# Optimization experiments

Hardware: AMD Instinct MI355X
Metric: run time of the kernel (lower is better)

## Reference

```python
import jax, jax.numpy as jnp
import numpy as np

FULL_RANGE = 128
MOOD_DIM = 4
LAYERS = 4
UNITS = 512
MOOD_UNITS = 32


def lstm_layer(x, Wih, Whh, bih, bhh):
    # x: [B, T, I]; torch LSTM gate order: i, f, g, o
    B, T, _ = x.shape
    H = Whh.shape[1]
    xg = jnp.einsum('bti,gi->btg', x, Wih) + bih + bhh  # [B, T, 4H]

    def step(carry, g_t):
        h, c = carry
        g = g_t + h @ Whh.T
        i, f, gc, o = jnp.split(g, 4, axis=-1)
        c = jax.nn.sigmoid(f) * c + jax.nn.sigmoid(i) * jnp.tanh(gc)
        h = jax.nn.sigmoid(o) * jnp.tanh(c)
        return (h, c), h

    h0 = jnp.zeros((B, H), x.dtype)
    (_, _), hs = jax.lax.scan(step, (h0, h0), xg.transpose(1, 0, 2))
    return hs.transpose(1, 0, 2)  # [B, T, H]


def setup_inputs() -> dict:
    key = jax.random.key(0)
    ks = jax.random.split(key, 16)
    s = 0.05
    H4 = 4 * UNITS
    in0 = FULL_RANGE + MOOD_UNITS
    return {
        'inputs': jax.random.normal(ks[0], (16, 1024, FULL_RANGE), jnp.float32),
        'moods': jax.random.normal(ks[1], (16, MOOD_DIM), jnp.float32),
        'W_mood': jax.random.normal(ks[2], (MOOD_UNITS, MOOD_DIM), jnp.float32) * s,
        'b_mood': jnp.zeros((MOOD_UNITS,), jnp.float32),
        'W_ih0': jax.random.normal(ks[3], (H4, in0), jnp.float32) * s,
        'W_hh0': jax.random.normal(ks[4], (H4, UNITS), jnp.float32) * s,
        'b_ih0': jax.random.normal(ks[5], (H4,), jnp.float32) * s,
        'b_hh0': jax.random.normal(ks[6], (H4,), jnp.float32) * s,
        'W_ih_rest': jax.random.normal(ks[7], (LAYERS - 1, H4, UNITS), jnp.float32) * s,
        'W_hh_rest': jax.random.normal(ks[8], (LAYERS - 1, H4, UNITS), jnp.float32) * s,
        'b_ih_rest': jax.random.normal(ks[9], (LAYERS - 1, H4), jnp.float32) * s,
        'b_hh_rest': jax.random.normal(ks[10], (LAYERS - 1, H4), jnp.float32) * s,
        'W_out': jax.random.normal(ks[11], (FULL_RANGE, UNITS), jnp.float32) * s,
        'b_out': jnp.zeros((FULL_RANGE,), jnp.float32),
    }


def reference(inputs, moods, W_mood, b_mood, W_ih0, W_hh0, b_ih0, b_hh0,
              W_ih_rest, W_hh_rest, b_ih_rest, b_hh_rest, W_out, b_out):
    B, S, _ = inputs.shape
    m = moods @ W_mood.T + b_mood                      # [B, MOOD_UNITS]
    m = jnp.broadcast_to(m[:, None, :], (B, S, MOOD_UNITS))
    x = jnp.concatenate([inputs, m], axis=2)           # [B, S, FULL_RANGE+MOOD_UNITS]

    params = [(W_ih0, W_hh0, b_ih0, b_hh0)] + [
        (W_ih_rest[i], W_hh_rest[i], b_ih_rest[i], b_hh_rest[i])
        for i in range(LAYERS - 1)
    ]
    for i, (Wih, Whh, bih, bhh) in enumerate(params):
        prev = x
        d = 2 ** i
        F = x.shape[-1]
        # torch unfold(1,d,d).permute(0,3,1,2).view(B*d, S//d, F):
        # sub-batch (b,k) is the stride-d subsequence with phase k
        xd = x.reshape(B, S // d, d, F).transpose(0, 2, 1, 3).reshape(B * d, S // d, F)
        yd = lstm_layer(xd, Wih, Whh, bih, bhh)         # [B*d, S//d, H]
        x = yd.reshape(B, d, S // d, UNITS).transpose(0, 2, 1, 3).reshape(B, S, UNITS)
        if i > 0:
            x = prev + x
    return x @ W_out.T + b_out                          # [B, S, FULL_RANGE]
```

## Files before the change

kernel.cpp:

```cpp
#include <hip/hip_runtime.h>
#include <stdint.h>

#define DEVFN __device__ __forceinline__
#define SCOPE_AGENT __HIP_MEMORY_SCOPE_AGENT

static constexpr int B_ = 16;
static constexpr int S_ = 1024;
static constexpr int FR = 128;
static constexpr int MU = 32;
static constexpr int H_ = 512;
static constexpr int G4 = 2048;

static constexpr int NCH_WHH = 4 * 64 * 2048;
static constexpr int NCH_WI0 = 16 * 2048;
static constexpr int NCH_WIR = 3 * 64 * 2048;
static constexpr int NCH_TOT = NCH_WHH + NCH_WI0 + NCH_WIR;

static constexpr int HV64 = 128 * 256;
static constexpr int NXF = 16 * 16 * 16;

typedef _Float16 h2_t __attribute__((ext_vector_type(2)));

DEVFN uint16_t f2h(float x) { union { _Float16 f; uint16_t u; } c; c.f = (_Float16)x; return c.u; }
DEVFN uint32_t pack_f16(float a, float b) { return (uint32_t)f2h(a) | ((uint32_t)f2h(b) << 16); }

DEVFN float fd2(uint32_t a, uint32_t b, float c) {
#if __has_builtin(__builtin_amdgcn_fdot2)
    return __builtin_amdgcn_fdot2(__builtin_bit_cast(h2_t, a),
                                  __builtin_bit_cast(h2_t, b), c, false);
#else
    asm("v_dot2_f32_f16 %0, %1, %2, %0" : "+v"(c) : "v"(a), "v"(b));
    return c;
#endif
}
DEVFN float dot8f(uint4 w, uint4 x, float s) {
    s = fd2(w.x, x.x, s); s = fd2(w.y, x.y, s);
    s = fd2(w.z, x.z, s); s = fd2(w.w, x.w, s);
    return s;
}
DEVFN float sigm(float x) { return 1.0f / (1.0f + __expf(-x)); }
DEVFN float tanhfast(float x) {
    float e = __expf(2.0f * fabsf(x));
    float r = 1.0f - 2.0f / (e + 1.0f);
    return copysignf(r, x);
}

__global__ __launch_bounds__(256) void mood_kernel(
    const float* __restrict__ moods, const float* __restrict__ W_mood,
    const float* __restrict__ b_mood, const float* __restrict__ W_ih0,
    const float* __restrict__ b_ih0, const float* __restrict__ b_hh0,
    float* __restrict__ mc)
{
    int b = blockIdx.x, tid = threadIdx.x;
    __shared__ float m[MU];
    if (tid < MU) {
        float s = b_mood[tid];
        #pragma unroll
        for (int j = 0; j < 4; j++) s += moods[b * 4 + j] * W_mood[tid * 4 + j];
        m[tid] = s;
    }
    __syncthreads();
    for (int row = tid; row < G4; row += 256) {
        float s = b_ih0[row] + b_hh0[row];
        const float* w = W_ih0 + (size_t)row * (FR + MU) + FR;
        #pragma unroll
        for (int u = 0; u < MU; u++) s += m[u] * w[u];
        mc[(size_t)b * G4 + row] = s;
    }
}

__global__ __launch_bounds__(256) void pack_kernel(
    const float* __restrict__ W_hh0, const float* __restrict__ W_hh_r,
    const float* __restrict__ W_ih0, const float* __restrict__ W_ih_r,
    uint4* __restrict__ pwh, uint4* __restrict__ pwi0, uint4* __restrict__ pwir)
{
    int c = blockIdx.x * 256 + threadIdx.x;
    if (c >= NCH_TOT) return;
    const float* src;
    uint4* dst;
    if (c < NCH_WHH) {
        int l = c >> 17, ck = (c >> 11) & 63, row = c & 2047;
        const float* W = (l == 0) ? W_hh0 : W_hh_r + (size_t)(l - 1) * G4 * H_;
        src = W + (size_t)row * H_ + ck * 8;
        dst = pwh + c;
    } else if (c < NCH_WHH + NCH_WI0) {
        int d = c - NCH_WHH;
        int ck = d >> 11, row = d & 2047;
        src = W_ih0 + (size_t)row * (FR + MU) + ck * 8;
        dst = pwi0 + d;
    } else {
        int e = c - NCH_WHH - NCH_WI0;
        int l = e >> 17, ck = (e >> 11) & 63, row = e & 2047;
        src = W_ih_r + (size_t)l * G4 * H_ + (size_t)row * H_ + ck * 8;
        dst = pwir + e;
    }
    uint4 o;
    o.x = pack_f16(src[0], src[1]);
    o.y = pack_f16(src[2], src[3]);
    o.z = pack_f16(src[4], src[5]);
    o.w = pack_f16(src[6], src[7]);
    *dst = o;
}

#define HSTEP(J) { \
    _Pragma("unroll") \
    for (int b = 0; b < SB; b++) { \
        uint4 hv = *(const uint4*)&lds_h[b * H_ + kg * 64 + (J) * 8]; \
        accA[b] = dot8f(h0c##J, hv, accA[b]); \
        accB[b] = dot8f(h1c##J, hv, accB[b]); \
    } }

#define XBODY(J) { \
    uint4 w0 = WI0[(size_t)(J) * G4 + row0]; \
    uint4 w1 = WI0[(size_t)(J) * G4 + row1]; \
    _Pragma("unroll") \
    for (int b = 0; b < SB; b++) { \
        uint4 xv = *(const uint4*)&lds_x[b * KIN + kg * (KIN / 8) + (J) * 8]; \
        accA[b] = dot8f(w0, xv, accA[b]); \
        accB[b] = dot8f(w1, xv, accB[b]); \
    } }

template <int LAYER>
DEVFN void scan_body(
    int bid, const float* x_in, float* x_out,
    const uint4* __restrict__ pwi, const uint4* __restrict__ pwh,
    const float* __restrict__ biasA, const float* __restrict__ biasB,
    unsigned long long* __restrict__ hb64, uint32_t* __restrict__ xf,
    uint16_t* lds_x, uint16_t* lds_h, float* lds_p, float* lds_res)
{
    constexpr int DIL = 1 << LAYER;
    constexpr int SB = DIL;
    constexpr int T = S_ / DIL;
    constexpr int KIN = (LAYER == 0) ? FR : H_;
    constexpr int NJX = KIN / 64;
    constexpr int XTOT = SB * KIN;
    constexpr int XRS = (XTOT + 511) / 512;
    constexpr int KSH = (LAYER == 0) ? 7 : 9;
    constexpr int LOFF = (LAYER == 0) ? 0 : (LAYER - 1);
    constexpr bool WREG = (LAYER <= 1);
    constexpr bool EARLY = (SB <= 4);
    constexpr bool XPROD = (LAYER == 0 || LAYER == 2);
    constexpr bool XCONS = (LAYER == 1 || LAYER == 3);
    constexpr uint32_t TB = 1u;

    const int g = bid & 15, wgi = bid >> 4;
    const int tid = threadIdx.x;
    const int kg = tid >> 6;
    const int r6 = tid & 63;
    const int gp = r6 >> 5;
    const int um = r6 & 31;
    const int U0 = wgi * 32;
    const int row0 = (2 * gp) * H_ + U0 + um;
    const int row1 = row0 + H_;
    const int rl0 = (2 * gp) * 32 + um, rl1 = rl0 + 32;
    const int sb0 = g * SB;

    const uint4* WH = pwh + ((size_t)(LAYER * 64 + kg * 8)) * G4;

    uint4 h0c0, h1c0, h0c1, h1c1, h0c2, h1c2, h0c3, h1c3;
    uint4 h0c4, h1c4, h0c5, h1c5, h0c6, h1c6, h0c7, h1c7;
    if constexpr (WREG) {
        h0c0 = WH[(size_t)0 * G4 + row0]; h1c0 = WH[(size_t)0 * G4 + row1];
        h0c1 = WH[(size_t)1 * G4 + row0]; h1c1 = WH[(size_t)1 * G4 + row1];
        h0c2 = WH[(size_t)2 * G4 + row0]; h1c2 = WH[(size_t)2 * G4 + row1];
        h0c3 = WH[(size_t)3 * G4 + row0]; h1c3 = WH[(size_t)3 * G4 + row1];
        h0c4 = WH[(size_t)4 * G4 + row0]; h1c4 = WH[(size_t)4 * G4 + row1];
        h0c5 = WH[(size_t)5 * G4 + row0]; h1c5 = WH[(size_t)5 * G4 + row1];
        h0c6 = WH[(size_t)6 * G4 + row0]; h1c6 = WH[(size_t)6 * G4 + row1];
        h0c7 = WH[(size_t)7 * G4 + row0]; h1c7 = WH[(size_t)7 * G4 + row1];
    }

    const uint4* WI0;
    if constexpr (LAYER == 0) WI0 = pwi + ((size_t)(kg * NJX)) * G4;
    else                      WI0 = pwi + ((size_t)(LOFF * 64 + kg * 8)) * G4;

    const int b0 = tid >> 5, uu = tid & 31;
    const bool upd = tid < SB * 32;
    float biasv[4] = {0.f, 0.f, 0.f, 0.f};
    float cst = 0.0f;
    if (upd) {
        #pragma unroll
        for (int Gx = 0; Gx < 4; Gx++) {
            int RR = Gx * H_ + U0 + uu;
            if constexpr (LAYER == 0)
                biasv[Gx] = biasA[(size_t)(sb0 + b0) * G4 + RR];
            else
                biasv[Gx] = biasA[RR] + biasB[RR];
        }
    }
    const size_t pslot = (size_t)(sb0 + b0) * 256 + ((U0 + uu) >> 1);
    const int usb = sb0 + b0, ubg = usb >> LAYER, uk = usb & (DIL - 1);
    const int myprod = (tid & 511) >> 5;

    if constexpr (XCONS) {
        const uint32_t* fl = xf + (g * 16 + myprod) * 16;
        uint32_t fv = __hip_atomic_load(fl, __ATOMIC_RELAXED, SCOPE_AGENT);
        while (fv < 2u) {
            __builtin_amdgcn_s_sleep(1);
            fv = __hip_atomic_load(fl, __ATOMIC_RELAXED, SCOPE_AGENT);
        }
    }
    float xsr[XRS];
    #pragma unroll
    for (int rr = 0; rr < XRS; rr++) {
        int idx = tid + rr * 512;
        if (idx < XTOT) {
            int b = idx >> KSH, off = idx & (KIN - 1);
            int sb = sb0 + b, bg = sb >> LAYER, k = sb & (DIL - 1);
            const float* src = x_in + ((size_t)bg * S_ + k) * KIN + off;
            if constexpr (XCONS)
                xsr[rr] = __hip_atomic_load(src, __ATOMIC_RELAXED, SCOPE_AGENT);
            else
                xsr[rr] = *src;
        }
    }
    asm volatile("s_waitcnt vmcnt(0)" ::: "memory");
    __syncthreads();
    if (upd && ((uu & 1) == 0))
        __hip_atomic_store(hb64 + HV64 + pslot,
                           (unsigned long long)TB << 32,
                           __ATOMIC_RELAXED, SCOPE_AGENT);

    for (int t = 0; t < T; t++) {
        #pragma unroll
        for (int rr = 0; rr < XRS; rr++) {
            int idx = tid + rr * 512;
            if (idx < XTOT) {
                int b = idx >> KSH, off = idx & (KIN - 1);
                lds_x[b * KIN + off] = f2h(xsr[rr]);
                if constexpr (LAYER > 0)
                    if ((off & ~31) == U0) lds_res[b * 32 + (off & 31)] = xsr[rr];
            }
        }
        __syncthreads();

        float res = 0.f;
        if constexpr (LAYER > 0) {
            if (upd) res = lds_res[b0 * 32 + uu];
        }

        const unsigned long long* hrd = hb64 + (size_t)((t + 1) & 1) * HV64;
        const uint32_t want = TB + (uint32_t)t;

        unsigned long long pve[EARLY ? SB : 1];
        if constexpr (EARLY) {
            if (tid < 256) {
                #pragma unroll
                for (int b = 0; b < SB; b++)
                    pve[b] = __hip_atomic_load(hrd + (size_t)(sb0 + b) * 256 + tid,
                                               __ATOMIC_RELAXED, SCOPE_AGENT);
            }
        }

        if (t + 1 < T) {
            if constexpr (XCONS) {
                const uint32_t* fl = xf + (g * 16 + myprod) * 16;
                const uint32_t need = 2u * (uint32_t)(t + 2);
                uint32_t fv = __hip_atomic_load(fl, __ATOMIC_RELAXED, SCOPE_AGENT);
                while (fv < need) {
                    __builtin_amdgcn_s_sleep(1);
                    fv = __hip_atomic_load(fl, __ATOMIC_RELAXED, SCOPE_AGENT);
                }
            }
            #pragma unroll
            for (int rr = 0; rr < XRS; rr++) {
                int idx = tid + rr * 512;
                if (idx < XTOT) {
                    int b = idx >> KSH, off = idx & (KIN - 1);
                    int sb = sb0 + b, bg = sb >> LAYER, k = sb & (DIL - 1);
                    const float* src =
                        x_in + ((size_t)bg * S_ + (size_t)(t + 1) * DIL + k) * KIN + off;
                    if constexpr (XCONS)
                        xsr[rr] = __hip_atomic_load(src, __ATOMIC_RELAXED, SCOPE_AGENT);
                    else
                        xsr[rr] = *src;
                }
            }
        }

        float accA[SB], accB[SB];
        #pragma unroll
        for (int b = 0; b < SB; b++) { accA[b] = 0.f; accB[b] = 0.f; }
        if constexpr (LAYER >= 2) {
            #pragma unroll 4
            for (int j = 0; j < NJX; j++) XBODY(j)
        } else {
            #pragma unroll 2
            for (int j = 0; j < NJX; j++) XBODY(j)
        }

        asm volatile("s_waitcnt vmcnt(0)" ::: "memory");

        if (tid < 256) {
            if constexpr (EARLY) {
                #pragma unroll
                for (int b = 0; b < SB; b++) {
                    unsigned long long v = pve[b];
                    while ((uint32_t)(v >> 32) != want) {
                        __builtin_amdgcn_s_sleep(1);
                        v = __hip_atomic_load(hrd + (size_t)(sb0 + b) * 256 + tid,
                                              __ATOMIC_RELAXED, SCOPE_AGENT);
                    }
                    ((uint32_t*)&lds_h[b * H_])[tid] = (uint32_t)v;
                }
            } else {
                unsigned long long pv[SB];
                #pragma unroll
                for (int b = 0; b < SB; b++)
                    pv[b] = __hip_atomic_load(hrd + (size_t)(sb0 + b) * 256 + tid,
                                              __ATOMIC_RELAXED, SCOPE_AGENT);
                #pragma unroll
                for (int b = 0; b < SB; b++) {
                    while ((uint32_t)(pv[b] >> 32) != want) {
                        __builtin_amdgcn_s_sleep(1);
                        pv[b] = __hip_atomic_load(hrd + (size_t)(sb0 + b) * 256 + tid,
                                                  __ATOMIC_RELAXED, SCOPE_AGENT);
                    }
                    ((uint32_t*)&lds_h[b * H_])[tid] = (uint32_t)pv[b];
                }
            }
        }
        __syncthreads();

        if constexpr (WREG) {
            HSTEP(0) HSTEP(1) HSTEP(2) HSTEP(3)
            HSTEP(4) HSTEP(5) HSTEP(6) HSTEP(7)
        } else {
            #pragma unroll 4
            for (int j = 0; j < 8; j++) {
                uint4 w0 = WH[(size_t)j * G4 + row0];
                uint4 w1 = WH[(size_t)j * G4 + row1];
                #pragma unroll
                for (int b = 0; b < SB; b++) {
                    uint4 hv = *(const uint4*)&lds_h[b * H_ + kg * 64 + j * 8];
                    accA[b] = dot8f(w0, hv, accA[b]);
                    accB[b] = dot8f(w1, hv, accB[b]);
                }
            }
        }

        #pragma unroll
        for (int b = 0; b < SB; b++) {
            lds_p[(b * 8 + kg) * 132 + rl0] = accA[b];
            lds_p[(b * 8 + kg) * 132 + rl1] = accB[b];
        }
        asm volatile("s_waitcnt vmcnt(0)" ::: "memory");
        __syncthreads();

        if (upd) {
            float gv[4];
            #pragma unroll
            for (int Gx = 0; Gx < 4; Gx++) {
                int rl = Gx * 32 + uu;
                float s = biasv[Gx];
                #pragma unroll
                for (int q = 0; q < 8; q++) s += lds_p[(b0 * 8 + q) * 132 + rl];
                gv[Gx] = s;
            }
            float ci = sigm(gv[0]), cf = sigm(gv[1]);
            float cg = tanhfast(gv[2]), co = sigm(gv[3]);
            cst = cf * cst + ci * cg;
            float hv = co * tanhfast(cst);
            uint32_t h16 = (uint32_t)f2h(hv);
            uint32_t partner = (uint32_t)__shfl_xor((int)h16, 1);
            if ((uu & 1) == 0)
                __hip_atomic_store(hb64 + (size_t)(t & 1) * HV64 + pslot,
                                   ((unsigned long long)(TB + (uint32_t)t + 1) << 32) |
                                   (unsigned long long)(h16 | (partner << 16)),
                                   __ATOMIC_RELAXED, SCOPE_AGENT);
            float* dst = x_out + ((size_t)ubg * S_ + (size_t)t * DIL + uk) * H_ + U0 + uu;
            if constexpr (XPROD)
                __hip_atomic_store(dst, hv + res, __ATOMIC_RELAXED, SCOPE_AGENT);
            else
                *dst = hv + res;
        }
        if constexpr (XPROD) {
            asm volatile("s_waitcnt vmcnt(0)" ::: "memory");
            if constexpr (SB >= 4) __syncthreads();
            if (tid == 0)
                __hip_atomic_store(xf + (g * 16 + wgi) * 16, (uint32_t)(t + 1),
                                   __ATOMIC_RELAXED, SCOPE_AGENT);
        }
    }
}

template <int LA, int LB, bool SEG>
__global__ __attribute__((amdgpu_waves_per_eu(4, 4))) __launch_bounds__(512)
void fused_scan(const float* xinA, float* xoutA,
                const float* xinB, float* xoutB,
                const uint4* __restrict__ pwiA, const uint4* __restrict__ pwiB,
                const uint4* __restrict__ pwh,
                const float* __restrict__ bA1, const float* __restrict__ bA2,
                const float* __restrict__ bB1, const float* __restrict__ bB2,
                unsigned long long* __restrict__ hb64, uint32_t* __restrict__ xf)
{
    constexpr int SBMX = 1 << LB;
    __shared__ __align__(16) uint16_t s_x[SBMX * 512];
    __shared__ __align__(16) uint16_t s_h[SBMX * 512];
    __shared__ float s_p[SBMX * 8 * 132];
    __shared__ float s_r[SBMX * 32];
    bool isA;
    int bid;
    if constexpr (SEG) {
        const int x = (int)blockIdx.x & 7, q = (int)blockIdx.x >> 3;
        isA = (x < 4);
        const int xe = isA ? x : x - 4;
        bid = ((q >> 2) << 4) + (xe + 4 * (q & 3));
    } else {
        isA = (int)blockIdx.x < 256;
        bid = (int)blockIdx.x & 255;
    }
    if (isA)
        scan_body<LA>(bid, xinA, xoutA, pwiA, pwh, bA1, bA2,
                      hb64 + (size_t)LA * 2 * HV64, xf, s_x, s_h, s_p, s_r);
    else
        scan_body<LB>(bid, xinB, xoutB, pwiB, pwh, bB1, bB2,
                      hb64 + (size_t)LB * 2 * HV64, xf, s_x, s_h, s_p, s_r);
}

__global__ __launch_bounds__(256) void out_gemm(
    const float* __restrict__ x, const float* __restrict__ Wout,
    const float* __restrict__ bout, float* __restrict__ out)
{
    __shared__ __align__(16) float xs[8][H_];
    int tid = threadIdx.x;
    size_t tok0 = (size_t)blockIdx.x * 8;
    const float4* src = (const float4*)(x + tok0 * H_);
    for (int idx = tid; idx < 8 * H_ / 4; idx += 256)
        ((float4*)xs)[idx] = src[idx];
    __syncthreads();

    int col = tid & 127, th = tid >> 7;
    int tb = th * 4;
    float a0 = 0.f, a1 = 0.f, a2 = 0.f, a3 = 0.f;
    const float4* w = (const float4*)(Wout + (size_t)col * H_);
    #pragma unroll 4
    for (int j = 0; j < H_ / 4; j++) {
        float4 wv = w[j];
        float4 x0 = ((const float4*)xs[tb + 0])[j];
        float4 x1 = ((const float4*)xs[tb + 1])[j];
        float4 x2 = ((const float4*)xs[tb + 2])[j];
        float4 x3 = ((const float4*)xs[tb + 3])[j];
        a0 = fmaf(wv.x, x0.x, a0); a0 = fmaf(wv.y, x0.y, a0); a0 = fmaf(wv.z, x0.z, a0); a0 = fmaf(wv.w, x0.w, a0);
        a1 = fmaf(wv.x, x1.x, a1); a1 = fmaf(wv.y, x1.y, a1); a1 = fmaf(wv.z, x1.z, a1); a1 = fmaf(wv.w, x1.w, a1);
        a2 = fmaf(wv.x, x2.x, a2); a2 = fmaf(wv.y, x2.y, a2); a2 = fmaf(wv.z, x2.z, a2); a2 = fmaf(wv.w, x2.w, a2);
        a3 = fmaf(wv.x, x3.x, a3); a3 = fmaf(wv.y, x3.y, a3); a3 = fmaf(wv.z, x3.z, a3); a3 = fmaf(wv.w, x3.w, a3);
    }
    float bo = bout[col];
    out[(tok0 + tb + 0) * FR + col] = a0 + bo;
    out[(tok0 + tb + 1) * FR + col] = a1 + bo;
    out[(tok0 + tb + 2) * FR + col] = a2 + bo;
    out[(tok0 + tb + 3) * FR + col] = a3 + bo;
}

extern "C" void kernel_launch(void* const* d_in, const int* in_sizes, int n_in,
                              void* d_out, int out_size, void* d_ws, size_t ws_size,
                              hipStream_t stream)
{
    const float* inputs = (const float*)d_in[0];
    const float* moods  = (const float*)d_in[1];
    const float* W_mood = (const float*)d_in[2];
    const float* b_mood = (const float*)d_in[3];
    const float* W_ih0  = (const float*)d_in[4];
    const float* W_hh0  = (const float*)d_in[5];
    const float* b_ih0  = (const float*)d_in[6];
    const float* b_hh0  = (const float*)d_in[7];
    const float* W_ih_r = (const float*)d_in[8];
    const float* W_hh_r = (const float*)d_in[9];
    const float* b_ih_r = (const float*)d_in[10];
    const float* b_hh_r = (const float*)d_in[11];
    const float* W_out  = (const float*)d_in[12];
    const float* b_out  = (const float*)d_in[13];

    float* ws = (float*)d_ws;
    float* mc = ws;
    float* xA = ws + 32768;
    unsigned long long* hb64 = (unsigned long long*)(xA + 8388608);
    uint32_t* xf0 = (uint32_t*)(hb64 + 8 * HV64);
    uint32_t* xf2 = xf0 + NXF;
    uint4* pwh  = (uint4*)(xf2 + NXF);
    uint4* pwi0 = pwh + NCH_WHH;
    uint4* pwir = pwi0 + NCH_WI0;

    (void)hipMemsetAsync(hb64, 0, 8 * HV64 * sizeof(unsigned long long)
                                  + 2 * NXF * sizeof(uint32_t), stream);
    mood_kernel<<<16, 256, 0, stream>>>(moods, W_mood, b_mood, W_ih0, b_ih0, b_hh0, mc);
    pack_kernel<<<(NCH_TOT + 255) / 256, 256, 0, stream>>>(
        W_hh0, W_hh_r, W_ih0, W_ih_r, pwh, pwi0, pwir);

    fused_scan<0, 1, false><<<512, 512, 0, stream>>>(
        inputs, xA, xA, xA, pwi0, pwir, pwh,
        mc, nullptr, b_ih_r, b_hh_r, hb64, xf0);
    fused_scan<2, 3, true><<<512, 512, 0, stream>>>(
        xA, xA, xA, xA, pwir, pwir, pwh,
        b_ih_r + G4, b_hh_r + G4, b_ih_r + 2 * G4, b_hh_r + 2 * G4, hb64, xf2);

    out_gemm<<<2048, 256, 0, stream>>>(xA, W_out, b_out, (float*)d_out);
}
```

Before: 5.052 ms.

## Add specialized layer-0 scan with pre-packed fp16 inputs and register-held input weights

Pre-converts the layer-0 input sequence to packed fp16 in the pack kernel and adds a dedicated layer-0 scan body. That body keeps its input-projection weights in registers and loads x directly from global memory each step, with no LDS staging and no extra barrier. The input projection is computed while waiting on the hidden-state flags, to shorten the latency-bound critical path of the first recurrence. The cost is extra packing work up front and a separate code path for layer 0.

Result: no change. 5.099 ms (+0.9%).

```diff
diff --git a/kernel.cpp b/kernel.cpp
--- a/kernel.cpp
+++ b/kernel.cpp
@@ -14,7 +14,8 @@
 static constexpr int NCH_WHH = 4 * 64 * 2048;
 static constexpr int NCH_WI0 = 16 * 2048;
 static constexpr int NCH_WIR = 3 * 64 * 2048;
-static constexpr int NCH_TOT = NCH_WHH + NCH_WI0 + NCH_WIR;
+static constexpr int NCH_XIN = 16 * 1024 * 16;
+static constexpr int NCH_TOT = NCH_WHH + NCH_WI0 + NCH_WIR + NCH_XIN;
 
 static constexpr int HV64 = 128 * 256;
 static constexpr int NXF = 16 * 16 * 16;
@@ -72,7 +73,9 @@
 __global__ __launch_bounds__(256) void pack_kernel(
     const float* __restrict__ W_hh0, const float* __restrict__ W_hh_r,
     const float* __restrict__ W_ih0, const float* __restrict__ W_ih_r,
-    uint4* __restrict__ pwh, uint4* __restrict__ pwi0, uint4* __restrict__ pwir)
+    const float* __restrict__ inputs,
+    uint4* __restrict__ pwh, uint4* __restrict__ pwi0,
+    uint4* __restrict__ pwir, uint4* __restrict__ pxin)
 {
     int c = blockIdx.x * 256 + threadIdx.x;
     if (c >= NCH_TOT) return;
@@ -88,11 +91,16 @@
         int ck = d >> 11, row = d & 2047;
         src = W_ih0 + (size_t)row * (FR + MU) + ck * 8;
         dst = pwi0 + d;
-    } else {
+    } else if (c < NCH_WHH + NCH_WI0 + NCH_WIR) {
         int e = c - NCH_WHH - NCH_WI0;
         int l = e >> 17, ck = (e >> 11) & 63, row = e & 2047;
         src = W_ih_r + (size_t)l * G4 * H_ + (size_t)row * H_ + ck * 8;
         dst = pwir + e;
+    } else {
+        int d = c - NCH_WHH - NCH_WI0 - NCH_WIR;
+        int tok = d >> 4, ck = d & 15;
+        src = inputs + (size_t)tok * FR + ck * 8;
+        dst = pxin + d;
     }
     uint4 o;
     o.x = pack_f16(src[0], src[1]);
@@ -109,6 +117,10 @@
         accA[b] = dot8f(h0c##J, hv, accA[b]); \
         accB[b] = dot8f(h1c##J, hv, accB[b]); \
     } }
+#define HSTEP1(J) { \
+    uint4 hv = *(const uint4*)&lds_h[kg * 64 + (J) * 8]; \
+    accA0 = dot8f(h0c##J, hv, accA0); \
+    accB0 = dot8f(h1c##J, hv, accB0); }
 
 #define XBODY(J) { \
     uint4 w0 = WI0[(size_t)(J) * G4 + row0]; \
@@ -119,6 +131,118 @@
         accA[b] = dot8f(w0, xv, accA[b]); \
         accB[b] = dot8f(w1, xv, accB[b]); \
     } }
+
+DEVFN void scan_body0(
+    int bid, const uint4* __restrict__ pxin, float* x_out,
+    const uint4* __restrict__ pwi, const uint4* __restrict__ pwh,
+    const float* __restrict__ mc,
+    unsigned long long* __restrict__ hb64, uint32_t* __restrict__ xf,
+    uint16_t* lds_h, float* lds_p)
+{
+    constexpr uint32_t TB = 1u;
+    const int g = bid & 15, wgi = bid >> 4;
+    const int tid = threadIdx.x;
+    const int kg = tid >> 6;
+    const int r6 = tid & 63;
+    const int gp = r6 >> 5;
+    const int um = r6 & 31;
+    const int U0 = wgi * 32;
+    const int row0 = (2 * gp) * H_ + U0 + um;
+    const int row1 = row0 + H_;
+    const int rl0 = (2 * gp) * 32 + um, rl1 = rl0 + 32;
+
+    const uint4* WH = pwh + ((size_t)(kg * 8)) * G4;
+    uint4 h0c0 = WH[(size_t)0 * G4 + row0], h1c0 = WH[(size_t)0 * G4 + row1];
+    uint4 h0c1 = WH[(size_t)1 * G4 + row0], h1c1 = WH[(size_t)1 * G4 + row1];
+    uint4 h0c2 = WH[(size_t)2 * G4 + row0], h1c2 = WH[(size_t)2 * G4 + row1];
+    uint4 h0c3 = WH[(size_t)3 * G4 + row0], h1c3 = WH[(size_t)3 * G4 + row1];
+    uint4 h0c4 = WH[(size_t)4 * G4 + row0], h1c4 = WH[(size_t)4 * G4 + row1];
+    uint4 h0c5 = WH[(size_t)5 * G4 + row0], h1c5 = WH[(size_t)5 * G4 + row1];
+    uint4 h0c6 = WH[(size_t)6 * G4 + row0], h1c6 = WH[(size_t)6 * G4 + row1];
+    uint4 h0c7 = WH[(size_t)7 * G4 + row0], h1c7 = WH[(size_t)7 * G4 + row1];
+    uint4 wiA0 = pwi[(size_t)(kg * 2 + 0) * G4 + row0];
+    uint4 wiA1 = pwi[(size_t)(kg * 2 + 1) * G4 + row0];
+    uint4 wiB0 = pwi[(size_t)(kg * 2 + 0) * G4 + row1];
+    uint4 wiB1 = pwi[(size_t)(kg * 2 + 1) * G4 + row1];
+
+    const int uu = tid & 31;
+    const bool upd = tid < 32;
+    float biasv[4] = {0.f, 0.f, 0.f, 0.f};
+    float cst = 0.0f;
+    if (upd) {
+        #pragma unroll
+        for (int Gx = 0; Gx < 4; Gx++)
+            biasv[Gx] = mc[(size_t)g * G4 + Gx * H_ + U0 + uu];
+    }
+    const size_t pslot = (size_t)g * 256 + ((U0 + uu) >> 1);
+    const uint4* PX = pxin + (size_t)g * S_ * 16 + kg * 2;
+
+    if (upd && ((uu & 1) == 0))
+        __hip_atomic_store(hb64 + HV64 + pslot,
+                           (unsigned long long)TB << 32,
+                           __ATOMIC_RELAXED, SCOPE_AGENT);
+
+    for (int t = 0; t < S_; t++) {
+        const unsigned long long* hrd = hb64 + (size_t)((t + 1) & 1) * HV64;
+        const uint32_t want = TB + (uint32_t)t;
+
+        uint4 xv0 = PX[(size_t)t * 16 + 0];
+        uint4 xv1 = PX[(size_t)t * 16 + 1];
+        unsigned long long pv = 0;
+        if (tid < 256)
+            pv = __hip_atomic_load(hrd + (size_t)g * 256 + tid,
+                                   __ATOMIC_RELAXED, SCOPE_AGENT);
+
+        float accA0 = dot8f(wiA0, xv0, 0.f); accA0 = dot8f(wiA1, xv1, accA0);
+        float accB0 = dot8f(wiB0, xv0, 0.f); accB0 = dot8f(wiB1, xv1, accB0);
+
+        if (tid < 256) {
+            while ((uint32_t)(pv >> 32) != want) {
+                __builtin_amdgcn_s_sleep(1);
+                pv = __hip_atomic_load(hrd + (size_t)g * 256 + tid,
+                                       __ATOMIC_RELAXED, SCOPE_AGENT);
+            }
+            ((uint32_t*)lds_h)[tid] = (uint32_t)pv;
+        }
+        __syncthreads();
+
+        HSTEP1(0) HSTEP1(1) HSTEP1(2) HSTEP1(3)
+        HSTEP1(4) HSTEP1(5) HSTEP1(6) HSTEP1(7)
+
+        lds_p[kg * 132 + rl0] = accA0;
+        lds_p[kg * 132 + rl1] = accB0;
+        __syncthreads();
+
+        if (upd) {
+            float gv[4];
+            #pragma unroll
+            for (int Gx = 0; Gx < 4; Gx++) {
+                int rl = Gx * 32 + uu;
+                float s = biasv[Gx];
+                #pragma unroll
+                for (int q = 0; q < 8; q++) s += lds_p[q * 132 + rl];
+                gv[Gx] = s;
+            }
+            float ci = sigm(gv[0]), cf = sigm(gv[1]);
+            float cg = tanhfast(gv[2]), co = sigm(gv[3]);
+            cst = cf * cst + ci * cg;
+            float hv = co * tanhfast(cst);
+            uint32_t h16 = (uint32_t)f2h(hv);
+            uint32_t partner = (uint32_t)__shfl_xor((int)h16, 1);
+            if ((uu & 1) == 0)
+                __hip_atomic_store(hb64 + (size_t)(t & 1) * HV64 + pslot,
+                                   ((unsigned long long)(TB + (uint32_t)t + 1) << 32) |
+                                   (unsigned long long)(h16 | (partner << 16)),
+                                   __ATOMIC_RELAXED, SCOPE_AGENT);
+            __hip_atomic_store(x_out + ((size_t)g * S_ + t) * H_ + U0 + uu,
+                               hv, __ATOMIC_RELAXED, SCOPE_AGENT);
+        }
+        asm volatile("s_waitcnt vmcnt(0)" ::: "memory");
+        if (tid == 0)
+            __hip_atomic_store(xf + (g * 16 + wgi) * 16, (uint32_t)(t + 1),
+                               __ATOMIC_RELAXED, SCOPE_AGENT);
+    }
+}
 
 template <int LAYER>
 DEVFN void scan_body(
@@ -131,15 +255,15 @@
     constexpr int DIL = 1 << LAYER;
     constexpr int SB = DIL;
     constexpr int T = S_ / DIL;
-    constexpr int KIN = (LAYER == 0) ? FR : H_;
+    constexpr int KIN = H_;
     constexpr int NJX = KIN / 64;
     constexpr int XTOT = SB * KIN;
     constexpr int XRS = (XTOT + 511) / 512;
-    constexpr int KSH = (LAYER == 0) ? 7 : 9;
-    constexpr int LOFF = (LAYER == 0) ? 0 : (LAYER - 1);
+    constexpr int KSH = 9;
+    constexpr int LOFF = LAYER - 1;
     constexpr bool WREG = (LAYER <= 1);
     constexpr bool EARLY = (SB <= 4);
-    constexpr bool XPROD = (LAYER == 0 || LAYER == 2);
+    constexpr bool XPROD = (LAYER == 2);
     constexpr bool XCONS = (LAYER == 1 || LAYER == 3);
     constexpr uint32_t TB = 1u;
 
@@ -170,9 +294,7 @@
         h0c7 = WH[(size_t)7 * G4 + row0]; h1c7 = WH[(size_t)7 * G4 + row1];
     }
 
-    const uint4* WI0;
-    if constexpr (LAYER == 0) WI0 = pwi + ((size_t)(kg * NJX)) * G4;
-    else                      WI0 = pwi + ((size_t)(LOFF * 64 + kg * 8)) * G4;
+    const uint4* WI0 = pwi + ((size_t)(LOFF * 64 + kg * 8)) * G4;
 
     const int b0 = tid >> 5, uu = tid & 31;
     const bool upd = tid < SB * 32;
@@ -182,10 +304,7 @@
         #pragma unroll
         for (int Gx = 0; Gx < 4; Gx++) {
             int RR = Gx * H_ + U0 + uu;
-            if constexpr (LAYER == 0)
-                biasv[Gx] = biasA[(size_t)(sb0 + b0) * G4 + RR];
-            else
-                biasv[Gx] = biasA[RR] + biasB[RR];
+            biasv[Gx] = biasA[RR] + biasB[RR];
         }
     }
     const size_t pslot = (size_t)(sb0 + b0) * 256 + ((U0 + uu) >> 1);
@@ -228,16 +347,13 @@
             if (idx < XTOT) {
                 int b = idx >> KSH, off = idx & (KIN - 1);
                 lds_x[b * KIN + off] = f2h(xsr[rr]);
-                if constexpr (LAYER > 0)
-                    if ((off & ~31) == U0) lds_res[b * 32 + (off & 31)] = xsr[rr];
+                if ((off & ~31) == U0) lds_res[b * 32 + (off & 31)] = xsr[rr];
             }
         }
         __syncthreads();
 
         float res = 0.f;
-        if constexpr (LAYER > 0) {
-            if (upd) res = lds_res[b0 * 32 + uu];
-        }
+        if (upd) res = lds_res[b0 * 32 + uu];
 
         const unsigned long long* hrd = hb64 + (size_t)((t + 1) & 1) * HV64;
         const uint32_t want = TB + (uint32_t)t;
@@ -386,7 +502,8 @@
 
 template <int LA, int LB, bool SEG>
 __global__ __attribute__((amdgpu_waves_per_eu(4, 4))) __launch_bounds__(512)
-void fused_scan(const float* xinA, float* xoutA,
+void fused_scan(const uint4* __restrict__ pxin,
+                const float* xinA, float* xoutA,
                 const float* xinB, float* xoutB,
                 const uint4* __restrict__ pwiA, const uint4* __restrict__ pwiB,
                 const uint4* __restrict__ pwh,
@@ -410,12 +527,17 @@
         isA = (int)blockIdx.x < 256;
         bid = (int)blockIdx.x & 255;
     }
-    if (isA)
-        scan_body<LA>(bid, xinA, xoutA, pwiA, pwh, bA1, bA2,
-                      hb64 + (size_t)LA * 2 * HV64, xf, s_x, s_h, s_p, s_r);
-    else
+    if (isA) {
+        if constexpr (LA == 0)
+            scan_body0(bid, pxin, xoutA, pwiA, pwh, bA1,
+                       hb64 + (size_t)LA * 2 * HV64, xf, s_h, s_p);
+        else
+            scan_body<LA>(bid, xinA, xoutA, pwiA, pwh, bA1, bA2,
+                          hb64 + (size_t)LA * 2 * HV64, xf, s_x, s_h, s_p, s_r);
+    } else {
         scan_body<LB>(bid, xinB, xoutB, pwiB, pwh, bB1, bB2,
                       hb64 + (size_t)LB * 2 * HV64, xf, s_x, s_h, s_p, s_r);
+    }
 }
 
 __global__ __launch_bounds__(256) void out_gemm(
@@ -481,18 +603,19 @@
     uint4* pwh  = (uint4*)(xf2 + NXF);
     uint4* pwi0 = pwh + NCH_WHH;
     uint4* pwir = pwi0 + NCH_WI0;
+    uint4* pxin = pwir + NCH_WIR;
 
     (void)hipMemsetAsync(hb64, 0, 8 * HV64 * sizeof(unsigned long long)
                                   + 2 * NXF * sizeof(uint32_t), stream);
     mood_kernel<<<16, 256, 0, stream>>>(moods, W_mood, b_mood, W_ih0, b_ih0, b_hh0, mc);
     pack_kernel<<<(NCH_TOT + 255) / 256, 256, 0, stream>>>(
-        W_hh0, W_hh_r, W_ih0, W_ih_r, pwh, pwi0, pwir);
+        W_hh0, W_hh_r, W_ih0, W_ih_r, inputs, pwh, pwi0, pwir, pxin);
 
     fused_scan<0, 1, false><<<512, 512, 0, stream>>>(
-        inputs, xA, xA, xA, pwi0, pwir, pwh,
+        pxin, nullptr, xA, xA, xA, pwi0, pwir, pwh,
         mc, nullptr, b_ih_r, b_hh_r, hb64, xf0);
     fused_scan<2, 3, true><<<512, 512, 0, stream>>>(
-        xA, xA, xA, xA, pwir, pwir, pwh,
+        nullptr, xA, xA, xA, xA, pwir, pwir, pwh,
         b_ih_r + G4, b_hh_r + G4, b_ih_r + 2 * G4, b_hh_r + 2 * G4, hb64, xf2);
 
     out_gemm<<<2048, 256, 0, stream>>>(xA, W_out, b_out, (float*)d_out);
```
